# Kernel optimization log

Measured on AMD Instinct MI355X. Metric: run time of the kernel, lower is better.

## Reference

```python
import jax, jax.numpy as jnp
import numpy as np
from jax import lax

SCORE_THRESHOLD = 0.5
IOU_THRESHOLD = 0.5
IMG_SIZE = 640.0
SPLITTER_THRESHOLD = 0.0
N = 4096


def setup_inputs() -> dict:
    key = jax.random.key(0)
    # raw RT-DETR output: [1, N, 5] = (cx, cy, w, h, person_conf), all in [0, 1]
    rtdetr_raw_out = jax.random.uniform(key, (1, N, 5), dtype=jnp.float32)
    return {"rtdetr_raw_out": rtdetr_raw_out}


def _iou_matrix(boxes):
    # boxes: [N, 4] in xyxy. Returns [N, N] pairwise IoU.
    x1, y1, x2, y2 = boxes[:, 0], boxes[:, 1], boxes[:, 2], boxes[:, 3]
    area = (x2 - x1) * (y2 - y1)  # [N]
    ix1 = jnp.maximum(x1[:, None], x1[None, :])
    iy1 = jnp.maximum(y1[:, None], y1[None, :])
    ix2 = jnp.minimum(x2[:, None], x2[None, :])
    iy2 = jnp.minimum(y2[:, None], y2[None, :])
    iw = jnp.clip(ix2 - ix1, 0.0)
    ih = jnp.clip(iy2 - iy1, 0.0)
    inter = iw * ih
    union = area[:, None] + area[None, :] - inter
    return inter / jnp.maximum(union, 1e-9)


def reference(rtdetr_raw_out):
    raw = rtdetr_raw_out[0]  # squeeze(0) -> [N, 5]
    conf = raw[:, 4]
    # splitter: keep boxes with conf > 0.0 (expressed as a mask for fixed shapes)
    valid = conf > SPLITTER_THRESHOLD
    # cxcywh scaled to pixel coords, then converted to xyxy
    cxcywh = raw[:, :4] * IMG_SIZE
    cx, cy, w, h = cxcywh[:, 0], cxcywh[:, 1], cxcywh[:, 2], cxcywh[:, 3]
    xyxy = jnp.stack([cx - w * 0.5, cy - h * 0.5, cx + w * 0.5, cy + h * 0.5], axis=1)
    # NMS score filter: conf >= score_threshold
    valid = valid & (conf >= SCORE_THRESHOLD)
    # sort by score descending; invalid boxes sink to the bottom with -inf keys
    sort_key = jnp.where(valid, conf, -jnp.inf)
    order = jnp.argsort(-sort_key)
    boxes_s = xyxy[order]          # [N, 4]
    conf_s = conf[order]           # [N]
    valid_s = valid[order]         # [N]
    iou = _iou_matrix(boxes_s)     # [N, N]
    idx = jnp.arange(N)

    def body(i, keep):
        keep_i = keep[i]
        # suppress any lower-ranked box with IoU > threshold to a kept box i
        sup = (iou[i] > IOU_THRESHOLD) & keep_i & (idx > i)
        return keep & (~sup)

    keep = lax.fori_loop(0, N, body, valid_s)
    boxes_and_scores = jnp.concatenate([boxes_s, conf_s[:, None]], axis=1)  # [N, 5]
    # fixed-shape equivalent of boolean-gather: suppressed/invalid rows zeroed
    return boxes_and_scores * keep[:, None].astype(boxes_and_scores.dtype)
```

## Files before the change

kernel.cpp:

```cpp
#include <hip/hip_runtime.h>
#include <stdint.h>

#define NBOX 4096
#define IMG 640.0f

typedef unsigned long long u64;
typedef unsigned int u32;


__global__ __launch_bounds__(256) void k_rank(const float* __restrict__ raw,
                                              int* __restrict__ rank_partial, int* __restrict__ Mp) {
    const int bi = blockIdx.x, bj = blockIdx.y;
    const int t = threadIdx.x;
    const int i = bi * 256 + t;
    if (bi == 0 && bj == 0 && t == 0) *Mp = 0;
    __shared__ float cj[256];
    cj[t] = raw[(bj * 256 + t) * 5 + 4];
    __syncthreads();

    const float ci = raw[i * 5 + 4];
    const int jbase = bj * 256;
    int rank = 0;
    const float4* c4 = reinterpret_cast<const float4*>(cj);
#pragma unroll 4
    for (int j4 = 0; j4 < 64; ++j4) {
        float4 c = c4[j4];
        int j = jbase + j4 * 4;
        rank += (c.x > ci || (c.x == ci && (j + 0) < i)) ? 1 : 0;
        rank += (c.y > ci || (c.y == ci && (j + 1) < i)) ? 1 : 0;
        rank += (c.z > ci || (c.z == ci && (j + 2) < i)) ? 1 : 0;
        rank += (c.w > ci || (c.w == ci && (j + 3) < i)) ? 1 : 0;
    }
    rank_partial[bj * NBOX + i] = rank;
}

__global__ __launch_bounds__(256) void k_scatter(const float* __restrict__ raw,
                                                 const int* __restrict__ rank_partial,
                                                 float* __restrict__ sx1, float* __restrict__ sy1,
                                                 float* __restrict__ sx2, float* __restrict__ sy2,
                                                 float* __restrict__ sconf, int* __restrict__ Mp) {
    const int i = blockIdx.x * 256 + threadIdx.x;
    const float ci = raw[i * 5 + 4];
    const bool vi = (ci >= 0.5f);

    int rank = 0;
#pragma unroll
    for (int k = 0; k < 16; ++k) rank += rank_partial[k * NBOX + i];

    u64 bal = __ballot(vi);
    if ((threadIdx.x & 63) == 0) atomicAdd(Mp, (int)__popcll(bal));

    if (vi) {
        float cx = __fmul_rn(raw[i * 5 + 0], IMG);
        float cy = __fmul_rn(raw[i * 5 + 1], IMG);
        float w  = __fmul_rn(raw[i * 5 + 2], IMG);
        float h  = __fmul_rn(raw[i * 5 + 3], IMG);
        float hw = __fmul_rn(w, 0.5f);
        float hh = __fmul_rn(h, 0.5f);
        sx1[rank]   = __fsub_rn(cx, hw);
        sy1[rank]   = __fsub_rn(cy, hh);
        sx2[rank]   = __fadd_rn(cx, hw);
        sy2[rank]   = __fadd_rn(cy, hh);
        sconf[rank] = ci;
    }
}

__global__ __launch_bounds__(256) void k_mask(const float* __restrict__ sx1, const float* __restrict__ sy1,
                                              const float* __restrict__ sx2, const float* __restrict__ sy2,
                                              const int* __restrict__ Mp,
                                              u64* __restrict__ mask, u64* __restrict__ diagR) {
    const int w = blockIdx.y;
    const int r = blockIdx.x * 256 + threadIdx.x;
    const int t = threadIdx.x;
    const int M = *Mp;

    __shared__ float cx1[64], cy1[64], cx2[64], cy2[64], car[64];
    if (t < 64) {
        int j = (w << 6) + t;
        float a1 = sx1[j], b1 = sy1[j], a2 = sx2[j], b2 = sy2[j];
        cx1[t] = a1; cy1[t] = b1; cx2[t] = a2; cy2[t] = b2;
        car[t] = __fmul_rn(__fsub_rn(a2, a1), __fsub_rn(b2, b1));
    }
    __syncthreads();

    u64 bits = 0ULL;
    if (r < M) {
        const float x1 = sx1[r], y1 = sy1[r], x2 = sx2[r], y2 = sy2[r];
        const float area_i = __fmul_rn(__fsub_rn(x2, x1), __fsub_rn(y2, y1));
        const int bmax = min(64, M - (w << 6));
        const int bmin = max(0, r + 1 - (w << 6));
        for (int b = bmin; b < bmax; ++b) {
            float xx1 = fmaxf(x1, cx1[b]);
            float yy1 = fmaxf(y1, cy1[b]);
            float xx2 = fminf(x2, cx2[b]);
            float yy2 = fminf(y2, cy2[b]);
            float iw = fmaxf(__fsub_rn(xx2, xx1), 0.0f);
            float ih = fmaxf(__fsub_rn(yy2, yy1), 0.0f);
            float inter = __fmul_rn(iw, ih);
            float uni = __fsub_rn(__fadd_rn(area_i, car[b]), inter);
            float iou = __fdiv_rn(inter, fmaxf(uni, 1e-9f));
            if (iou > 0.5f) bits |= (1ULL << b);
        }
        mask[((size_t)r << 6) + w] = bits;
    }

    if ((r >> 6) == w) diagR[r] = bits;
}

__global__ __launch_bounds__(576) void k_scan(const int* __restrict__ Mp,
                                              const u64* __restrict__ mask,
                                              const u64* __restrict__ diagR,
                                              const float* __restrict__ sx1, const float* __restrict__ sy1,
                                              const float* __restrict__ sx2, const float* __restrict__ sy2,
                                              const float* __restrict__ sconf,
                                              float* __restrict__ out) {
    __shared__ u64 remvArr[64];
    __shared__ u64 kbArr[64];
    const int tid = threadIdx.x;
    const int wave = tid >> 6;
    const int lane = tid & 63;
    const int M = *Mp;
    const int nblk = (M + 63) >> 6;

    if (tid < 64) { remvArr[tid] = 0ULL; kbArr[tid] = 0ULL; }

    if (nblk > 0) {
        if (wave == 0) {
            __builtin_amdgcn_s_setprio(1);
            u64 rv = diagR[lane];
            u32 rlo = (u32)rv, rhi = (u32)(rv >> 32);
            u64 cv = (nblk > 1) ? mask[((size_t)lane << 6) + 1] : 0ULL;
            u32 clo = (u32)cv, chi = (u32)(cv >> 32);
            u64 carry = 0ULL;

            for (int b = 0; b < nblk; ++b) {
                u64 rb = remvArr[b];
                const int rem = M - (b << 6);
                const u64 valid = (rem >= 64) ? ~0ULL : ((1ULL << rem) - 1ULL);
                u64 alive = valid & ~(rb | carry);
                u64 kb = 0ULL, car = 0ULL;
                while (alive) {
                    int i = __builtin_ctzll(alive);
                    alive &= alive - 1;
                    kb |= (1ULL << i);
                    u32 lo = __builtin_amdgcn_readlane(rlo, i);
                    u32 hi = __builtin_amdgcn_readlane(rhi, i);
                    u32 cl = __builtin_amdgcn_readlane(clo, i);
                    u32 ch = __builtin_amdgcn_readlane(chi, i);
                    alive &= ~(((u64)hi << 32) | (u64)lo);
                    car |= (((u64)ch << 32) | (u64)cl);
                }
                carry = car;
                if (lane == 0) kbArr[b] = kb;

                if (b + 1 < nblk) {
                    u64 nrv = diagR[((b + 1) << 6) + lane];
                    rlo = (u32)nrv; rhi = (u32)(nrv >> 32);
                    u64 ncv = (b + 2 < nblk)
                            ? mask[(((size_t)(b + 1) << 6) + lane) * 64 + (b + 2)]
                            : 0ULL;
                    clo = (u32)ncv; chi = (u32)(ncv >> 32);
                }
                asm volatile("s_waitcnt lgkmcnt(0)" ::: "memory");
                __builtin_amdgcn_s_barrier();
                __builtin_amdgcn_sched_barrier(0);
            }
        } else {
            const int w1 = wave - 1;
            const int slot = tid & 7;
            const int chunk = (tid >> 3) & 7;
            u64 v[8];
            for (int b = 0; b < nblk; ++b) {
                if (b >= 1) {
                    const u64 kb = kbArr[b - 1];
                    const int W = b + 1 + (w1 << 3) + slot;
                    if (kb != 0ULL && W < 64) {
                        u64 acc = 0ULL;
#pragma unroll
                        for (int k = 0; k < 8; ++k) {
                            const int r = chunk + (k << 3);
                            acc |= (((kb >> r) & 1ULL) ? v[k] : 0ULL);
                        }
                        acc |= __shfl_xor(acc, 8);
                        acc |= __shfl_xor(acc, 16);
                        acc |= __shfl_xor(acc, 32);
                        if (chunk == 0) remvArr[W] |= acc;
                    }
                }
                if (b + 1 < nblk) {
                    const int W2 = b + 2 + (w1 << 3) + slot;
                    const int Wc = (W2 < 64) ? W2 : 63;
                    const u64* rowbase = mask + ((size_t)b << 12);
#pragma unroll
                    for (int k = 0; k < 8; ++k) {
                        const int r = chunk + (k << 3);
                        v[k] = rowbase[((size_t)r << 6) + Wc];
                    }
                }
                asm volatile("s_waitcnt lgkmcnt(0)" ::: "memory");
                __builtin_amdgcn_s_barrier();
                __builtin_amdgcn_sched_barrier(0);
            }
        }
    }
    if (nblk == 0) __builtin_amdgcn_s_barrier();
    for (int g = tid; g < NBOX * 5; g += 576) {
        const int r = g / 5;
        const int c = g - r * 5;
        bool kept = false;
        if (r < M) kept = ((kbArr[r >> 6] >> (r & 63)) & 1ULL) != 0ULL;
        float vv = 0.0f;
        if (kept) {
            const float* arr = (c == 0) ? sx1 : (c == 1) ? sy1 : (c == 2) ? sx2 : (c == 3) ? sy2 : sconf;
            vv = arr[r];
        }
        out[g] = vv;
    }
}

extern "C" void kernel_launch(void* const* d_in, const int* in_sizes, int n_in,
                              void* d_out, int out_size, void* d_ws, size_t ws_size,
                              hipStream_t stream) {
    const float* raw = (const float*)d_in[0];
    char* ws = (char*)d_ws;
    float* sx1 = (float*)(ws + 0);
    float* sy1 = (float*)(ws + 16384);
    float* sx2 = (float*)(ws + 32768);
    float* sy2 = (float*)(ws + 49152);
    float* sconf = (float*)(ws + 65536);
    int* Mp = (int*)(ws + 81920);
    u64* diagR = (u64*)(ws + 86016);
    u64* mask = (u64*)(ws + 131072);
    int* rank_partial = (int*)(ws + 2228224);
    float* out = (float*)d_out;

    k_rank<<<dim3(16, 16), dim3(256), 0, stream>>>(raw, rank_partial, Mp);
    k_scatter<<<dim3(16), dim3(256), 0, stream>>>(raw, rank_partial, sx1, sy1, sx2, sy2, sconf, Mp);
    k_mask<<<dim3(16, 64), dim3(256), 0, stream>>>(sx1, sy1, sx2, sy2, Mp, mask, diagR);
    k_scan<<<dim3(1), dim3(576), 0, stream>>>(Mp, mask, diagR, sx1, sy1, sx2, sy2, sconf, out);
}
```

Before: 87.40 us.

## Transpose NMS mask layout and add prefetch wave staging scan inputs in LDS

The IoU bitmask is now stored column-major (word-block major), so each word block's rows are contiguous. Helper waves can then read coalesced runs instead of strided 512-byte hops, and the shuffle reduction is remapped to match. A new tenth wave prefetches the diagonal and carry mask words several blocks ahead into a 4-deep LDS ring. This takes global-load latency off the serial critical wave. The cost is an extra wave per barrier, more LDS, and the k_mask stores becoming strided.

```diff
diff --git a/kernel.cpp b/kernel.cpp
--- a/kernel.cpp
+++ b/kernel.cpp
@@ -68,7 +68,7 @@
 __global__ __launch_bounds__(256) void k_mask(const float* __restrict__ sx1, const float* __restrict__ sy1,
                                               const float* __restrict__ sx2, const float* __restrict__ sy2,
                                               const int* __restrict__ Mp,
-                                              u64* __restrict__ mask, u64* __restrict__ diagR) {
+                                              u64* __restrict__ maskT, u64* __restrict__ diagR) {
     const int w = blockIdx.y;
     const int r = blockIdx.x * 256 + threadIdx.x;
     const int t = threadIdx.x;
@@ -101,14 +101,14 @@
             float iou = __fdiv_rn(inter, fmaxf(uni, 1e-9f));
             if (iou > 0.5f) bits |= (1ULL << b);
         }
-        mask[((size_t)r << 6) + w] = bits;
+        maskT[((size_t)w << 12) + r] = bits;
     }
 
     if ((r >> 6) == w) diagR[r] = bits;
 }
 
-__global__ __launch_bounds__(576) void k_scan(const int* __restrict__ Mp,
-                                              const u64* __restrict__ mask,
+__global__ __launch_bounds__(640) void k_scan(const int* __restrict__ Mp,
+                                              const u64* __restrict__ maskT,
                                               const u64* __restrict__ diagR,
                                               const float* __restrict__ sx1, const float* __restrict__ sy1,
                                               const float* __restrict__ sx2, const float* __restrict__ sy2,
@@ -116,6 +116,8 @@
                                               float* __restrict__ out) {
     __shared__ u64 remvArr[64];
     __shared__ u64 kbArr[64];
+    __shared__ u64 dbuf[4][64];
+    __shared__ u64 cbuf[4][64];
     const int tid = threadIdx.x;
     const int wave = tid >> 6;
     const int lane = tid & 63;
@@ -125,11 +127,25 @@
     if (tid < 64) { remvArr[tid] = 0ULL; kbArr[tid] = 0ULL; }
 
     if (nblk > 0) {
+        if (wave == 9) {
+            u64 d0 = diagR[lane];
+            u64 c0 = maskT[(1ULL << 12) + lane];
+            u64 d1 = 0, c1 = 0;
+            if (1 < nblk) {
+                d1 = diagR[64 + lane];
+                c1 = maskT[(2ULL << 12) + 64 + lane];
+            }
+            dbuf[0][lane] = d0; cbuf[0][lane] = c0;
+            dbuf[1][lane] = d1; cbuf[1][lane] = c1;
+        }
+        asm volatile("s_waitcnt lgkmcnt(0)" ::: "memory");
+        __builtin_amdgcn_s_barrier();
+        __builtin_amdgcn_sched_barrier(0);
+
         if (wave == 0) {
             __builtin_amdgcn_s_setprio(1);
-            u64 rv = diagR[lane];
-            u32 rlo = (u32)rv, rhi = (u32)(rv >> 32);
-            u64 cv = (nblk > 1) ? mask[((size_t)lane << 6) + 1] : 0ULL;
+            u64 dv = dbuf[0][lane], cv = cbuf[0][lane];
+            u32 rlo = (u32)dv, rhi = (u32)(dv >> 32);
             u32 clo = (u32)cv, chi = (u32)(cv >> 32);
             u64 carry = 0ULL;
 
@@ -154,21 +170,40 @@
                 if (lane == 0) kbArr[b] = kb;
 
                 if (b + 1 < nblk) {
-                    u64 nrv = diagR[((b + 1) << 6) + lane];
-                    rlo = (u32)nrv; rhi = (u32)(nrv >> 32);
-                    u64 ncv = (b + 2 < nblk)
-                            ? mask[(((size_t)(b + 1) << 6) + lane) * 64 + (b + 2)]
-                            : 0ULL;
-                    clo = (u32)ncv; chi = (u32)(ncv >> 32);
+                    u64 nd = dbuf[(b + 1) & 3][lane];
+                    u64 nc = cbuf[(b + 1) & 3][lane];
+                    rlo = (u32)nd; rhi = (u32)(nd >> 32);
+                    clo = (u32)nc; chi = (u32)(nc >> 32);
                 }
                 asm volatile("s_waitcnt lgkmcnt(0)" ::: "memory");
                 __builtin_amdgcn_s_barrier();
                 __builtin_amdgcn_sched_barrier(0);
             }
+        } else if (wave == 9) {
+            u64 d_pend = 0, c_pend = 0;
+            if (2 < nblk) {
+                d_pend = diagR[(2 << 6) + lane];
+                c_pend = (3 < 64) ? maskT[(3ULL << 12) + (2 << 6) + lane] : 0ULL;
+            }
+            for (int b = 0; b < nblk; ++b) {
+                const int nb = b + 2;
+                if (nb < nblk) {
+                    dbuf[nb & 3][lane] = d_pend;
+                    cbuf[nb & 3][lane] = c_pend;
+                }
+                const int fb = b + 3;
+                if (fb < nblk) {
+                    d_pend = diagR[(fb << 6) + lane];
+                    c_pend = (fb + 1 < 64) ? maskT[((size_t)(fb + 1) << 12) + (fb << 6) + lane] : 0ULL;
+                }
+                asm volatile("s_waitcnt lgkmcnt(0)" ::: "memory");
+                __builtin_amdgcn_s_barrier();
+                __builtin_amdgcn_sched_barrier(0);
+            }
         } else {
             const int w1 = wave - 1;
-            const int slot = tid & 7;
-            const int chunk = (tid >> 3) & 7;
+            const int chunk = tid & 7;
+            const int slot = (tid >> 3) & 7;
             u64 v[8];
             for (int b = 0; b < nblk; ++b) {
                 if (b >= 1) {
@@ -181,21 +216,19 @@
                             const int r = chunk + (k << 3);
                             acc |= (((kb >> r) & 1ULL) ? v[k] : 0ULL);
                         }
-                        acc |= __shfl_xor(acc, 8);
-                        acc |= __shfl_xor(acc, 16);
-                        acc |= __shfl_xor(acc, 32);
+                        acc |= __shfl_xor(acc, 1);
+                        acc |= __shfl_xor(acc, 2);
+                        acc |= __shfl_xor(acc, 4);
                         if (chunk == 0) remvArr[W] |= acc;
                     }
                 }
                 if (b + 1 < nblk) {
                     const int W2 = b + 2 + (w1 << 3) + slot;
                     const int Wc = (W2 < 64) ? W2 : 63;
-                    const u64* rowbase = mask + ((size_t)b << 12);
+                    const u64* colbase = maskT + ((size_t)Wc << 12) + ((size_t)b << 6);
 #pragma unroll
-                    for (int k = 0; k < 8; ++k) {
-                        const int r = chunk + (k << 3);
-                        v[k] = rowbase[((size_t)r << 6) + Wc];
-                    }
+                    for (int k = 0; k < 8; ++k)
+                        v[k] = colbase[chunk + (k << 3)];
                 }
                 asm volatile("s_waitcnt lgkmcnt(0)" ::: "memory");
                 __builtin_amdgcn_s_barrier();
@@ -203,8 +236,11 @@
             }
         }
     }
-    if (nblk == 0) __builtin_amdgcn_s_barrier();
-    for (int g = tid; g < NBOX * 5; g += 576) {
+    if (nblk == 0) {
+        asm volatile("s_waitcnt lgkmcnt(0)" ::: "memory");
+        __builtin_amdgcn_s_barrier();
+    }
+    for (int g = tid; g < NBOX * 5; g += 640) {
         const int r = g / 5;
         const int c = g - r * 5;
         bool kept = false;
@@ -230,12 +266,12 @@
     float* sconf = (float*)(ws + 65536);
     int* Mp = (int*)(ws + 81920);
     u64* diagR = (u64*)(ws + 86016);
-    u64* mask = (u64*)(ws + 131072);
+    u64* maskT = (u64*)(ws + 131072);
     int* rank_partial = (int*)(ws + 2228224);
     float* out = (float*)d_out;
 
     k_rank<<<dim3(16, 16), dim3(256), 0, stream>>>(raw, rank_partial, Mp);
     k_scatter<<<dim3(16), dim3(256), 0, stream>>>(raw, rank_partial, sx1, sy1, sx2, sy2, sconf, Mp);
-    k_mask<<<dim3(16, 64), dim3(256), 0, stream>>>(sx1, sy1, sx2, sy2, Mp, mask, diagR);
-    k_scan<<<dim3(1), dim3(576), 0, stream>>>(Mp, mask, diagR, sx1, sy1, sx2, sy2, sconf, out);
-}
+    k_mask<<<dim3(16, 64), dim3(256), 0, stream>>>(sx1, sy1, sx2, sy2, Mp, maskT, diagR);
+    k_scan<<<dim3(1), dim3(640), 0, stream>>>(Mp, maskT, diagR, sx1, sy1, sx2, sy2, sconf, out);
+}
```

After: 79.81 us. -8.7%, faster.

## Collapse NMS scan into single-wave loop with register-held suppression vector

Applied to the files above, without the earlier changes.

Replaces the multi-wave producer/consumer scan, which used a barrier per 64-box block and shared-memory OR-reductions, with a single wave. That wave keeps the removed-bit vector in registers and, after each block, ORs the mask rows of the kept boxes, loading eight rows at a time. This removes the per-block barriers and the LDS traffic but serializes the mask-row gathers on one wave. The block size drops to 256 threads, so fewer threads remain for the final output write.

```diff
diff --git a/kernel.cpp b/kernel.cpp
--- a/kernel.cpp
+++ b/kernel.cpp
@@ -107,104 +107,77 @@
     if ((r >> 6) == w) diagR[r] = bits;
 }
 
-__global__ __launch_bounds__(576) void k_scan(const int* __restrict__ Mp,
+__global__ __launch_bounds__(256) void k_scan(const int* __restrict__ Mp,
                                               const u64* __restrict__ mask,
                                               const u64* __restrict__ diagR,
                                               const float* __restrict__ sx1, const float* __restrict__ sy1,
                                               const float* __restrict__ sx2, const float* __restrict__ sy2,
                                               const float* __restrict__ sconf,
                                               float* __restrict__ out) {
-    __shared__ u64 remvArr[64];
     __shared__ u64 kbArr[64];
     const int tid = threadIdx.x;
-    const int wave = tid >> 6;
     const int lane = tid & 63;
     const int M = *Mp;
     const int nblk = (M + 63) >> 6;
 
-    if (tid < 64) { remvArr[tid] = 0ULL; kbArr[tid] = 0ULL; }
-
-    if (nblk > 0) {
-        if (wave == 0) {
-            __builtin_amdgcn_s_setprio(1);
-            u64 rv = diagR[lane];
-            u32 rlo = (u32)rv, rhi = (u32)(rv >> 32);
-            u64 cv = (nblk > 1) ? mask[((size_t)lane << 6) + 1] : 0ULL;
-            u32 clo = (u32)cv, chi = (u32)(cv >> 32);
-            u64 carry = 0ULL;
-
-            for (int b = 0; b < nblk; ++b) {
-                u64 rb = remvArr[b];
-                const int rem = M - (b << 6);
-                const u64 valid = (rem >= 64) ? ~0ULL : ((1ULL << rem) - 1ULL);
-                u64 alive = valid & ~(rb | carry);
-                u64 kb = 0ULL, car = 0ULL;
-                while (alive) {
-                    int i = __builtin_ctzll(alive);
-                    alive &= alive - 1;
-                    kb |= (1ULL << i);
-                    u32 lo = __builtin_amdgcn_readlane(rlo, i);
-                    u32 hi = __builtin_amdgcn_readlane(rhi, i);
-                    u32 cl = __builtin_amdgcn_readlane(clo, i);
-                    u32 ch = __builtin_amdgcn_readlane(chi, i);
-                    alive &= ~(((u64)hi << 32) | (u64)lo);
-                    car |= (((u64)ch << 32) | (u64)cl);
-                }
-                carry = car;
-                if (lane == 0) kbArr[b] = kb;
-
-                if (b + 1 < nblk) {
-                    u64 nrv = diagR[((b + 1) << 6) + lane];
-                    rlo = (u32)nrv; rhi = (u32)(nrv >> 32);
-                    u64 ncv = (b + 2 < nblk)
-                            ? mask[(((size_t)(b + 1) << 6) + lane) * 64 + (b + 2)]
-                            : 0ULL;
-                    clo = (u32)ncv; chi = (u32)(ncv >> 32);
-                }
-                asm volatile("s_waitcnt lgkmcnt(0)" ::: "memory");
-                __builtin_amdgcn_s_barrier();
-                __builtin_amdgcn_sched_barrier(0);
+    if (tid < 64) kbArr[tid] = 0ULL;
+
+    if ((tid >> 6) == 0 && nblk > 0) {
+        __builtin_amdgcn_s_setprio(1);
+        u64 d = diagR[lane];
+        u32 dlo = (u32)d, dhi = (u32)(d >> 32);
+        u32 rvlo = 0, rvhi = 0;
+
+        for (int b = 0; b < nblk; ++b) {
+            u64 nd = (b + 1 < nblk) ? diagR[((b + 1) << 6) + lane] : 0ULL;
+
+            u32 rbl = (u32)__builtin_amdgcn_readlane(rvlo, b);
+            u32 rbh = (u32)__builtin_amdgcn_readlane(rvhi, b);
+            const u64 rb = ((u64)rbh << 32) | (u64)rbl;
+            const int rem = M - (b << 6);
+            const u64 valid = (rem >= 64) ? ~0ULL : ((1ULL << rem) - 1ULL);
+            u64 alive = valid & ~rb;
+            u64 kb = 0ULL;
+            while (alive) {
+                int i = __builtin_ctzll(alive);
+                alive &= alive - 1;
+                kb |= (1ULL << i);
+                u32 lo = (u32)__builtin_amdgcn_readlane(dlo, i);
+                u32 hi = (u32)__builtin_amdgcn_readlane(dhi, i);
+                alive &= ~(((u64)hi << 32) | (u64)lo);
             }
-        } else {
-            const int w1 = wave - 1;
-            const int slot = tid & 7;
-            const int chunk = (tid >> 3) & 7;
-            u64 v[8];
-            for (int b = 0; b < nblk; ++b) {
-                if (b >= 1) {
-                    const u64 kb = kbArr[b - 1];
-                    const int W = b + 1 + (w1 << 3) + slot;
-                    if (kb != 0ULL && W < 64) {
-                        u64 acc = 0ULL;
-#pragma unroll
-                        for (int k = 0; k < 8; ++k) {
-                            const int r = chunk + (k << 3);
-                            acc |= (((kb >> r) & 1ULL) ? v[k] : 0ULL);
-                        }
-                        acc |= __shfl_xor(acc, 8);
-                        acc |= __shfl_xor(acc, 16);
-                        acc |= __shfl_xor(acc, 32);
-                        if (chunk == 0) remvArr[W] |= acc;
-                    }
-                }
-                if (b + 1 < nblk) {
-                    const int W2 = b + 2 + (w1 << 3) + slot;
-                    const int Wc = (W2 < 64) ? W2 : 63;
-                    const u64* rowbase = mask + ((size_t)b << 12);
-#pragma unroll
-                    for (int k = 0; k < 8; ++k) {
-                        const int r = chunk + (k << 3);
-                        v[k] = rowbase[((size_t)r << 6) + Wc];
-                    }
-                }
-                asm volatile("s_waitcnt lgkmcnt(0)" ::: "memory");
-                __builtin_amdgcn_s_barrier();
-                __builtin_amdgcn_sched_barrier(0);
+            if (lane == 0) kbArr[b] = kb;
+
+            u64 t = kb;
+            const u64* rowbase = mask + ((size_t)(b << 6) << 6);
+            while (t) {
+                int i0 = __builtin_ctzll(t); t &= t - 1;
+                const bool h1 = t != 0ULL; int i1 = h1 ? __builtin_ctzll(t) : i0; if (h1) t &= t - 1;
+                const bool h2 = t != 0ULL; int i2 = h2 ? __builtin_ctzll(t) : i0; if (h2) t &= t - 1;
+                const bool h3 = t != 0ULL; int i3 = h3 ? __builtin_ctzll(t) : i0; if (h3) t &= t - 1;
+                const bool h4 = t != 0ULL; int i4 = h4 ? __builtin_ctzll(t) : i0; if (h4) t &= t - 1;
+                const bool h5 = t != 0ULL; int i5 = h5 ? __builtin_ctzll(t) : i0; if (h5) t &= t - 1;
+                const bool h6 = t != 0ULL; int i6 = h6 ? __builtin_ctzll(t) : i0; if (h6) t &= t - 1;
+                const bool h7 = t != 0ULL; int i7 = h7 ? __builtin_ctzll(t) : i0; if (h7) t &= t - 1;
+                u64 v0 = rowbase[((size_t)i0 << 6) + lane];
+                u64 v1 = rowbase[((size_t)i1 << 6) + lane];
+                u64 v2 = rowbase[((size_t)i2 << 6) + lane];
+                u64 v3 = rowbase[((size_t)i3 << 6) + lane];
+                u64 v4 = rowbase[((size_t)i4 << 6) + lane];
+                u64 v5 = rowbase[((size_t)i5 << 6) + lane];
+                u64 v6 = rowbase[((size_t)i6 << 6) + lane];
+                u64 v7 = rowbase[((size_t)i7 << 6) + lane];
+                u64 o = v0 | (h1 ? v1 : 0ULL) | (h2 ? v2 : 0ULL) | (h3 ? v3 : 0ULL)
+                           | (h4 ? v4 : 0ULL) | (h5 ? v5 : 0ULL) | (h6 ? v6 : 0ULL) | (h7 ? v7 : 0ULL);
+                rvlo |= (u32)o;
+                rvhi |= (u32)(o >> 32);
             }
+            dlo = (u32)nd; dhi = (u32)(nd >> 32);
         }
     }
-    if (nblk == 0) __builtin_amdgcn_s_barrier();
-    for (int g = tid; g < NBOX * 5; g += 576) {
+    __syncthreads();
+
+    for (int g = tid; g < NBOX * 5; g += 256) {
         const int r = g / 5;
         const int c = g - r * 5;
         bool kept = false;
@@ -237,5 +210,5 @@
     k_rank<<<dim3(16, 16), dim3(256), 0, stream>>>(raw, rank_partial, Mp);
     k_scatter<<<dim3(16), dim3(256), 0, stream>>>(raw, rank_partial, sx1, sy1, sx2, sy2, sconf, Mp);
     k_mask<<<dim3(16, 64), dim3(256), 0, stream>>>(sx1, sy1, sx2, sy2, Mp, mask, diagR);
-    k_scan<<<dim3(1), dim3(576), 0, stream>>>(Mp, mask, diagR, sx1, sy1, sx2, sy2, sconf, out);
-}
+    k_scan<<<dim3(1), dim3(256), 0, stream>>>(Mp, mask, diagR, sx1, sy1, sx2, sy2, sconf, out);
+}
```

After: 141.5 us. 61.9% more time.

## Transpose suppression mask and double-buffer scan prefetch with carry side array

Applied to the files above, without the earlier changes.

The IoU bitmask is now stored column-major (word-block major), so the helper waves in the serial scan read 8 contiguous rows of one column with coalesced loads instead of strided ones. The first off-diagonal carry word is written to a separate compact array, and the leader wave prefetches the diagonal and carry words three blocks ahead. Helper waves alternate between two register buffers, so mask loads for block b+2 are in flight while block b is folded, with the shuffle reduction axis remapped to match. The cost is an extra carry array and more registers per wave.

```diff
diff --git a/kernel.cpp b/kernel.cpp
--- a/kernel.cpp
+++ b/kernel.cpp
@@ -68,7 +68,8 @@
 __global__ __launch_bounds__(256) void k_mask(const float* __restrict__ sx1, const float* __restrict__ sy1,
                                               const float* __restrict__ sx2, const float* __restrict__ sy2,
                                               const int* __restrict__ Mp,
-                                              u64* __restrict__ mask, u64* __restrict__ diagR) {
+                                              u64* __restrict__ maskT, u64* __restrict__ diagR,
+                                              u64* __restrict__ carry1) {
     const int w = blockIdx.y;
     const int r = blockIdx.x * 256 + threadIdx.x;
     const int t = threadIdx.x;
@@ -101,15 +102,18 @@
             float iou = __fdiv_rn(inter, fmaxf(uni, 1e-9f));
             if (iou > 0.5f) bits |= (1ULL << b);
         }
-        mask[((size_t)r << 6) + w] = bits;
-    }
-
-    if ((r >> 6) == w) diagR[r] = bits;
+        maskT[((size_t)w << 12) + r] = bits;
+    }
+
+    const int rblk = r >> 6;
+    if (rblk == w)     diagR[r]  = bits;
+    if (rblk + 1 == w) carry1[r] = bits;
 }
 
 __global__ __launch_bounds__(576) void k_scan(const int* __restrict__ Mp,
-                                              const u64* __restrict__ mask,
+                                              const u64* __restrict__ maskT,
                                               const u64* __restrict__ diagR,
+                                              const u64* __restrict__ carry1,
                                               const float* __restrict__ sx1, const float* __restrict__ sy1,
                                               const float* __restrict__ sx2, const float* __restrict__ sy2,
                                               const float* __restrict__ sconf,
@@ -123,87 +127,103 @@
     const int nblk = (M + 63) >> 6;
 
     if (tid < 64) { remvArr[tid] = 0ULL; kbArr[tid] = 0ULL; }
+    __syncthreads();
 
     if (nblk > 0) {
         if (wave == 0) {
             __builtin_amdgcn_s_setprio(1);
-            u64 rv = diagR[lane];
-            u32 rlo = (u32)rv, rhi = (u32)(rv >> 32);
-            u64 cv = (nblk > 1) ? mask[((size_t)lane << 6) + 1] : 0ULL;
-            u32 clo = (u32)cv, chi = (u32)(cv >> 32);
+            u64 d0 = diagR[lane], e0 = carry1[lane];
+            u64 d1 = 0, e1 = 0, d2 = 0, e2 = 0;
+            if (1 < nblk) { d1 = diagR[64 + lane];  e1 = carry1[64 + lane];  }
+            if (2 < nblk) { d2 = diagR[128 + lane]; e2 = carry1[128 + lane]; }
             u64 carry = 0ULL;
 
             for (int b = 0; b < nblk; ++b) {
-                u64 rb = remvArr[b];
+                const u64 rb = remvArr[b] | carry;
                 const int rem = M - (b << 6);
                 const u64 valid = (rem >= 64) ? ~0ULL : ((1ULL << rem) - 1ULL);
-                u64 alive = valid & ~(rb | carry);
+                u64 alive = valid & ~rb;
                 u64 kb = 0ULL, car = 0ULL;
+                const u32 dlo = (u32)d0, dhi = (u32)(d0 >> 32);
+                const u32 el = (u32)e0, eh = (u32)(e0 >> 32);
                 while (alive) {
                     int i = __builtin_ctzll(alive);
                     alive &= alive - 1;
                     kb |= (1ULL << i);
-                    u32 lo = __builtin_amdgcn_readlane(rlo, i);
-                    u32 hi = __builtin_amdgcn_readlane(rhi, i);
-                    u32 cl = __builtin_amdgcn_readlane(clo, i);
-                    u32 ch = __builtin_amdgcn_readlane(chi, i);
+                    u32 lo = (u32)__builtin_amdgcn_readlane(dlo, i);
+                    u32 hi = (u32)__builtin_amdgcn_readlane(dhi, i);
+                    u32 p  = (u32)__builtin_amdgcn_readlane(el, i);
+                    u32 q  = (u32)__builtin_amdgcn_readlane(eh, i);
                     alive &= ~(((u64)hi << 32) | (u64)lo);
-                    car |= (((u64)ch << 32) | (u64)cl);
+                    car |= ((u64)q << 32) | (u64)p;
                 }
                 carry = car;
                 if (lane == 0) kbArr[b] = kb;
 
-                if (b + 1 < nblk) {
-                    u64 nrv = diagR[((b + 1) << 6) + lane];
-                    rlo = (u32)nrv; rhi = (u32)(nrv >> 32);
-                    u64 ncv = (b + 2 < nblk)
-                            ? mask[(((size_t)(b + 1) << 6) + lane) * 64 + (b + 2)]
-                            : 0ULL;
-                    clo = (u32)ncv; chi = (u32)(ncv >> 32);
-                }
+                d0 = d1; d1 = d2; e0 = e1; e1 = e2;
+                if (b + 3 < nblk) {
+                    d2 = diagR [((b + 3) << 6) + lane];
+                    e2 = carry1[((b + 3) << 6) + lane];
+                } else { d2 = 0ULL; e2 = 0ULL; }
+
                 asm volatile("s_waitcnt lgkmcnt(0)" ::: "memory");
                 __builtin_amdgcn_s_barrier();
                 __builtin_amdgcn_sched_barrier(0);
             }
         } else {
             const int w1 = wave - 1;
-            const int slot = tid & 7;
-            const int chunk = (tid >> 3) & 7;
-            u64 v[8];
-            for (int b = 0; b < nblk; ++b) {
-                if (b >= 1) {
-                    const u64 kb = kbArr[b - 1];
-                    const int W = b + 1 + (w1 << 3) + slot;
-                    if (kb != 0ULL && W < 64) {
-                        u64 acc = 0ULL;
-#pragma unroll
-                        for (int k = 0; k < 8; ++k) {
-                            const int r = chunk + (k << 3);
-                            acc |= (((kb >> r) & 1ULL) ? v[k] : 0ULL);
-                        }
-                        acc |= __shfl_xor(acc, 8);
-                        acc |= __shfl_xor(acc, 16);
-                        acc |= __shfl_xor(acc, 32);
-                        if (chunk == 0) remvArr[W] |= acc;
-                    }
+            const int chunk = tid & 7;
+            const int slot = (tid >> 3) & 7;
+            u64 vA[8], vB[8];
+
+#define ISSUE(DST, T)                                                          \
+    do {                                                                       \
+        const int W_ = (T) + 1 + (w1 << 3) + slot;                             \
+        const int Wc_ = (W_ < 64) ? W_ : 63;                                   \
+        const u64* cb_ = maskT + ((size_t)Wc_ << 12) + ((size_t)((T) - 1) << 6); \
+        _Pragma("unroll")                                                      \
+        for (int k = 0; k < 8; ++k) (DST)[k] = cb_[chunk + (k << 3)];          \
+    } while (0)
+
+#define FOLD(V, T)                                                             \
+    do {                                                                       \
+        const u64 kb_ = kbArr[(T) - 1];                                        \
+        const int W_ = (T) + 1 + (w1 << 3) + slot;                             \
+        if (W_ < 64 && kb_ != 0ULL) {                                          \
+            u64 acc_ = 0ULL;                                                   \
+            _Pragma("unroll")                                                  \
+            for (int k = 0; k < 8; ++k)                                        \
+                acc_ |= (((kb_ >> (chunk + (k << 3))) & 1ULL) ? (V)[k] : 0ULL); \
+            acc_ |= __shfl_xor(acc_, 1);                                       \
+            acc_ |= __shfl_xor(acc_, 2);                                       \
+            acc_ |= __shfl_xor(acc_, 4);                                       \
+            if (chunk == 0) remvArr[W_] |= acc_;                               \
+        }                                                                      \
+    } while (0)
+
+            if (1 < nblk) ISSUE(vA, 1);
+            for (int bb = 0; bb < nblk; bb += 2) {
+                {
+                    if (bb >= 2) FOLD(vB, bb);
+                    if (bb + 2 < nblk) ISSUE(vB, bb + 2);
+                    asm volatile("s_waitcnt lgkmcnt(0)" ::: "memory");
+                    __builtin_amdgcn_s_barrier();
+                    __builtin_amdgcn_sched_barrier(0);
                 }
-                if (b + 1 < nblk) {
-                    const int W2 = b + 2 + (w1 << 3) + slot;
-                    const int Wc = (W2 < 64) ? W2 : 63;
-                    const u64* rowbase = mask + ((size_t)b << 12);
-#pragma unroll
-                    for (int k = 0; k < 8; ++k) {
-                        const int r = chunk + (k << 3);
-                        v[k] = rowbase[((size_t)r << 6) + Wc];
-                    }
+                if (bb + 1 < nblk) {
+                    FOLD(vA, bb + 1);
+                    if (bb + 3 < nblk) ISSUE(vA, bb + 3);
+                    asm volatile("s_waitcnt lgkmcnt(0)" ::: "memory");
+                    __builtin_amdgcn_s_barrier();
+                    __builtin_amdgcn_sched_barrier(0);
                 }
-                asm volatile("s_waitcnt lgkmcnt(0)" ::: "memory");
-                __builtin_amdgcn_s_barrier();
-                __builtin_amdgcn_sched_barrier(0);
             }
+#undef ISSUE
+#undef FOLD
         }
     }
-    if (nblk == 0) __builtin_amdgcn_s_barrier();
+    __syncthreads();
+
     for (int g = tid; g < NBOX * 5; g += 576) {
         const int r = g / 5;
         const int c = g - r * 5;
@@ -229,13 +249,14 @@
     float* sy2 = (float*)(ws + 49152);
     float* sconf = (float*)(ws + 65536);
     int* Mp = (int*)(ws + 81920);
-    u64* diagR = (u64*)(ws + 86016);
-    u64* mask = (u64*)(ws + 131072);
-    int* rank_partial = (int*)(ws + 2228224);
+    u64* diagR  = (u64*)(ws + 86016);
+    u64* carry1 = (u64*)(ws + 118784);
+    u64* maskT = (u64*)(ws + 196608);
+    int* rank_partial = (int*)(ws + 2293760);
     float* out = (float*)d_out;
 
     k_rank<<<dim3(16, 16), dim3(256), 0, stream>>>(raw, rank_partial, Mp);
     k_scatter<<<dim3(16), dim3(256), 0, stream>>>(raw, rank_partial, sx1, sy1, sx2, sy2, sconf, Mp);
-    k_mask<<<dim3(16, 64), dim3(256), 0, stream>>>(sx1, sy1, sx2, sy2, Mp, mask, diagR);
-    k_scan<<<dim3(1), dim3(576), 0, stream>>>(Mp, mask, diagR, sx1, sy1, sx2, sy2, sconf, out);
-}
+    k_mask<<<dim3(16, 64), dim3(256), 0, stream>>>(sx1, sy1, sx2, sy2, Mp, maskT, diagR, carry1);
+    k_scan<<<dim3(1), dim3(576), 0, stream>>>(Mp, maskT, diagR, carry1, sx1, sy1, sx2, sy2, sconf, out);
+}
```

After: 90.33 us. 1.03x slower.
